# Performance work log

Measured on AMD Instinct MI355X. Metric: run time of the kernel, lower is better.

The kernel has to match this reference:

```python
import jax, jax.numpy as jnp
import numpy as np

IN_DIM = 128
OUT_DIM = 128
ATTN_DIM = 64
N_REL = 200
N_NODE = 50000
N_EDGE = 500000
N_QUERY = 64
COE_TIMEDIFF = 0.2  # computed in torch code but unused downstream


def setup_inputs() -> dict:
    key = jax.random.key(0)
    ks = jax.random.split(key, 24)
    # edges: [E,7] with columns (r_idx, _, rel, _, tau, sub, obj)
    r_idx = jax.random.randint(ks[0], (N_EDGE,), 0, N_QUERY)
    rel = jax.random.randint(ks[1], (N_EDGE,), 0, 2 * N_REL + 1)
    tau = jax.random.randint(ks[2], (N_EDGE,), -1, 366)  # -1 triggers the where() fallback
    sub = jax.random.randint(ks[3], (N_EDGE,), 0, N_NODE)
    obj = jax.random.randint(ks[4], (N_EDGE,), 0, N_NODE)
    fill = jnp.zeros((N_EDGE,), jnp.int64 if jax.config.jax_enable_x64 else jnp.int32)
    edges = jnp.stack([r_idx, fill, rel, fill, tau, sub, obj], axis=1)
    s = 1.0 / np.sqrt(IN_DIM)
    sa = 1.0 / np.sqrt(ATTN_DIM)
    return {
        "q_sub": jax.random.randint(ks[5], (N_QUERY,), 0, N_NODE),
        "q_rel": jax.random.randint(ks[6], (N_QUERY,), 0, 2 * N_REL + 1),
        "q_tau": jax.random.randint(ks[7], (N_QUERY,), 0, 366),
        "hidden": jax.random.normal(ks[8], (N_NODE, IN_DIM), jnp.float32),
        "edges": edges,
        "n_node": N_NODE,
        "old_nodes_new_idx": jax.random.randint(ks[9], (10000,), 0, N_NODE),
        "rela_embed": jax.random.normal(ks[10], (2 * N_REL + 1, IN_DIM), jnp.float32),
        "Ws": jax.random.normal(ks[11], (IN_DIM, ATTN_DIM), jnp.float32) * s,
        "Wr": jax.random.normal(ks[12], (IN_DIM, ATTN_DIM), jnp.float32) * s,
        "Wqr_W": jax.random.normal(ks[13], (IN_DIM, ATTN_DIM), jnp.float32) * s,
        "Wqr_b": jax.random.normal(ks[14], (ATTN_DIM,), jnp.float32) * s,
        "Wtau": jax.random.normal(ks[15], (IN_DIM, ATTN_DIM), jnp.float32) * s,
        "w_alpha_W": jax.random.normal(ks[16], (ATTN_DIM, 1), jnp.float32) * sa,
        "w_alpha_b": jax.random.normal(ks[17], (1,), jnp.float32) * sa,
        "Wh": jax.random.normal(ks[18], (IN_DIM, OUT_DIM), jnp.float32) * s,
        "wt1": jax.random.normal(ks[19], (1, IN_DIM), jnp.float32),
        "bt1": jax.random.normal(ks[20], (1, IN_DIM), jnp.float32),
        "wt2": jax.random.normal(ks[21], (1, IN_DIM), jnp.float32),
        "bt2": jax.random.normal(ks[22], (1, IN_DIM), jnp.float32),
    }


def reference(q_sub, q_rel, q_tau, hidden, edges, n_node, old_nodes_new_idx,
              rela_embed, Ws, Wr, Wqr_W, Wqr_b, Wtau, w_alpha_W, w_alpha_b,
              Wh, wt1, bt1, wt2, bt2):
    r_idx = edges[:, 0]
    rel = edges[:, 2]
    tau = edges[:, 4]
    sub = edges[:, 5]
    obj = edges[:, 6]
    hs = hidden[sub]                      # [E, in_dim] gather
    hr = rela_embed[rel]                  # [E, in_dim]
    h_qr = rela_embed[q_rel][r_idx]       # [E, in_dim]
    taus_q = q_tau[r_idx]
    tau = jnp.where(tau >= 0, tau, taus_q)
    delta_tau = (tau - taus_q).astype(hidden.dtype)[:, None]  # [E,1]
    h_tau = wt1 * delta_tau + bt1 + jnp.sin(wt2 * delta_tau + bt2)  # [E, in_dim]
    message = hs + hr + h_tau
    pre = jax.nn.relu(hs @ Ws + hr @ Wr + (h_qr @ Wqr_W + Wqr_b) + h_tau @ Wtau)
    alpha = jax.nn.sigmoid(pre @ w_alpha_W + w_alpha_b)  # [E,1]
    msg_agg = jax.ops.segment_sum(alpha * message, obj, num_segments=n_node)
    return msg_agg @ Wh  # act is identity by default
```

## Files before the change

kernel.cpp:

```cpp
#include <hip/hip_runtime.h>

#define IN_DIM   128
#define OUT_DIM  128
#define ATTN_DIM 64
#define N_RELV   401
#define N_NODE   50000
#define N_EDGE   500000
#define N_QUERY  64
#define N_DT     731
#define CAP      40

typedef unsigned short ushort_t;
typedef unsigned int   uint_t;
typedef __attribute__((ext_vector_type(8))) short v8s;
typedef __attribute__((ext_vector_type(4))) float v4f;

__device__ __forceinline__ int clampi(int v, int lo, int hi) {
    return v < lo ? lo : (v > hi ? hi : v);
}
__device__ __forceinline__ float bu2f(ushort_t u) {
    union { uint_t i; float f; } v; v.i = ((uint_t)u) << 16; return v.f;
}
__device__ __forceinline__ float blo(uint_t u) { return bu2f((ushort_t)(u & 0xffff)); }
__device__ __forceinline__ float bhi(uint_t u) { return bu2f((ushort_t)(u >> 16)); }
__device__ __forceinline__ ushort_t f2bu(float f) {
    union { float f; uint_t i; } v; v.f = f;
    const uint_t x = v.i;
    return (ushort_t)((x + 0x7fffu + ((x >> 16) & 1u)) >> 16);
}

__device__ __forceinline__ void parse_edge(const int* __restrict__ edges, int e,
                                           int i64, int& r, int& rel, int& tau,
                                           int& sub, int& obj) {
    if (i64) {
        const int* E = edges + (size_t)e * 14;
        r = E[0]; rel = E[4]; tau = E[8]; sub = E[10]; obj = E[12];
    } else {
        const int* E = edges + (size_t)e * 7;
        r = E[0]; rel = E[2]; tau = E[4]; sub = E[5]; obj = E[6];
    }
    r   = clampi(r,   0, N_QUERY - 1);
    rel = clampi(rel, 0, N_RELV - 1);
    sub = clampi(sub, 0, N_NODE - 1);
    obj = clampi(obj, 0, N_NODE - 1);
}

__global__ __launch_bounds__(256) void prep_kernel(
    const int* __restrict__ edges, const float* __restrict__ Ws,
    const float* __restrict__ Wh, ushort_t* __restrict__ WTb,
    int* __restrict__ flag, int* __restrict__ cnt, int* __restrict__ ovfn)
{
    const int i = blockIdx.x * 256 + threadIdx.x;
    const int n = i >> 7, k = i & 127;
    const float w = (n < 64) ? Ws[k * 64 + n] : Wh[k * 128 + (n - 64)];
    WTb[i] = f2bu(w);

    for (int idx = i; idx < N_NODE; idx += 96 * 256) cnt[idx] = 0;
    if (i == 0) ovfn[0] = 0;

    if (blockIdx.x == 0) {
        __shared__ int bad;
        if (threadIdx.x == 0) bad = 0;
        __syncthreads();
        for (int t = threadIdx.x; t < 1000; t += 256) {
            const int w32 = edges[2 * t + 1];
            if (w32 != 0 && w32 != -1) bad = 1;
        }
        __syncthreads();
        if (threadIdx.x == 0) flag[0] = (bad == 0) ? 1 : 0;
    }
}

__global__ __launch_bounds__(256) void node_tab_mfma(
    const float* __restrict__ hidden, const ushort_t* __restrict__ WTb,
    ushort_t* __restrict__ node_attn, ushort_t* __restrict__ node_msg)
{
    const int tid  = threadIdx.x;
    const int wid  = tid >> 6;
    const int lane = tid & 63;
    const int m16  = lane & 15;
    const int q    = lane >> 4;
    const int nb   = blockIdx.x * 64;
    const int row  = nb + wid * 16 + m16;
    const int rowc = row < N_NODE ? row : N_NODE - 1;

    v8s hfr[4];
    #pragma unroll
    for (int c = 0; c < 4; ++c) {
        const float4 f0 = *(const float4*)(hidden + (size_t)rowc * 128 + 32 * c + 8 * q);
        const float4 f1 = *(const float4*)(hidden + (size_t)rowc * 128 + 32 * c + 8 * q + 4);
        v8s a;
        a[0] = (short)f2bu(f0.x); a[1] = (short)f2bu(f0.y);
        a[2] = (short)f2bu(f0.z); a[3] = (short)f2bu(f0.w);
        a[4] = (short)f2bu(f1.x); a[5] = (short)f2bu(f1.y);
        a[6] = (short)f2bu(f1.z); a[7] = (short)f2bu(f1.w);
        hfr[c] = a;
    }

    #pragma unroll
    for (int t = 0; t < 12; ++t) {
        v4f acc = {0.f, 0.f, 0.f, 0.f};
        #pragma unroll
        for (int c = 0; c < 4; ++c) {
            const v8s wfr = *(const v8s*)(WTb + (size_t)(16 * t + m16) * 128 + 32 * c + 8 * q);
            acc = __builtin_amdgcn_mfma_f32_16x16x32_bf16(wfr, hfr[c], acc, 0, 0, 0);
        }
        if (row < N_NODE) {
            const uint_t u0 = (uint_t)f2bu(acc[0]) | ((uint_t)f2bu(acc[1]) << 16);
            const uint_t u1 = (uint_t)f2bu(acc[2]) | ((uint_t)f2bu(acc[3]) << 16);
            const int dim = 16 * t + 4 * q;
            if (dim < 64) {
                uint2* dst = (uint2*)(node_attn + (size_t)row * 64 + dim);
                *dst = make_uint2(u0, u1);
            } else {
                uint2* dst = (uint2*)(node_msg + (size_t)row * 128 + (dim - 64));
                *dst = make_uint2(u0, u1);
            }
        }
    }
}

__global__ __launch_bounds__(128) void tables_kernel(
    const float* __restrict__ rela, const float* __restrict__ Wr,
    const float* __restrict__ Wtau, const float* __restrict__ Wh,
    const float* __restrict__ wt1, const float* __restrict__ bt1,
    const float* __restrict__ wt2, const float* __restrict__ bt2,
    const int* __restrict__ q_rel, const float* __restrict__ WqrW,
    const float* __restrict__ Wqrb, const int* __restrict__ flag,
    ushort_t* __restrict__ rel_attn, ushort_t* __restrict__ rel_msg,
    ushort_t* __restrict__ dt_attn,  ushort_t* __restrict__ dt_msg,
    ushort_t* __restrict__ Xqr)
{
    const int b = blockIdx.x, tid = threadIdx.x;
    __shared__ float h[IN_DIM];

    if (b < N_RELV) {
        const int r = b;
        h[tid] = rela[(size_t)r * IN_DIM + tid];
        __syncthreads();
        if (tid < ATTN_DIM) {
            float a = 0.f;
            #pragma unroll 8
            for (int d = 0; d < IN_DIM; ++d) a += h[d] * Wr[d * ATTN_DIM + tid];
            rel_attn[(size_t)r * ATTN_DIM + tid] = f2bu(a);
        }
        float m = 0.f;
        #pragma unroll 8
        for (int d = 0; d < IN_DIM; ++d) m += h[d] * Wh[d * OUT_DIM + tid];
        rel_msg[(size_t)r * OUT_DIM + tid] = f2bu(m);
    } else if (b < N_RELV + N_DT) {
        const int i = b - N_RELV;
        const float dt = (float)(i - 365);
        h[tid] = wt1[tid] * dt + bt1[tid] + sinf(wt2[tid] * dt + bt2[tid]);
        __syncthreads();
        if (tid < ATTN_DIM) {
            float a = 0.f;
            #pragma unroll 8
            for (int d = 0; d < IN_DIM; ++d) a += h[d] * Wtau[d * ATTN_DIM + tid];
            dt_attn[(size_t)i * ATTN_DIM + tid] = f2bu(a);
        }
        float m = 0.f;
        #pragma unroll 8
        for (int d = 0; d < IN_DIM; ++d) m += h[d] * Wh[d * OUT_DIM + tid];
        dt_msg[(size_t)i * OUT_DIM + tid] = f2bu(m);
    } else {
        const int qn  = b - N_RELV - N_DT;
        const int i64 = flag[0];
        const int rel = clampi(q_rel[i64 ? 2 * qn : qn], 0, N_RELV - 1);
        h[tid] = rela[(size_t)rel * IN_DIM + tid];
        __syncthreads();
        if (tid < ATTN_DIM) {
            float acc = Wqrb[tid];
            #pragma unroll 8
            for (int d = 0; d < IN_DIM; ++d) acc += h[d] * WqrW[d * ATTN_DIM + tid];
            Xqr[(size_t)qn * ATTN_DIM + tid] = f2bu(acc);
        }
    }
}

__global__ __launch_bounds__(256) void alpha_scatter(
    const int* __restrict__ edges, const int* __restrict__ q_tau,
    const ushort_t* __restrict__ node_attn, const ushort_t* __restrict__ rel_attn,
    const ushort_t* __restrict__ dt_attn,  const ushort_t* __restrict__ Xqr,
    const float* __restrict__ w_alpha_W, const float* __restrict__ w_alpha_b,
    const int* __restrict__ flag, int* __restrict__ cnt,
    int4* __restrict__ meta, int* __restrict__ ovfn, int4* __restrict__ ovfl)
{
    const int g   = threadIdx.x & 7;
    const int e   = blockIdx.x * 32 + (threadIdx.x >> 3);
    const int i64 = flag[0];

    int r, rel, tau, sub, obj;
    parse_edge(edges, e, i64, r, rel, tau, sub, obj);
    const int tq = q_tau[i64 ? 2 * r : r];
    if (tau < 0) tau = tq;
    const int di = clampi(tau - tq + 365, 0, N_DT - 1);

    const uint4 xs = *(const uint4*)(node_attn + (size_t)sub * ATTN_DIM + 8 * g);
    const uint4 xr = *(const uint4*)(rel_attn + (size_t)rel * ATTN_DIM + 8 * g);
    const uint4 xt = *(const uint4*)(dt_attn  + (size_t)di  * ATTN_DIM + 8 * g);
    const uint4 xq = *(const uint4*)(Xqr      + (size_t)r   * ATTN_DIM + 8 * g);
    const float4 wA = *(const float4*)(w_alpha_W + 8 * g);
    const float4 wB = *(const float4*)(w_alpha_W + 8 * g + 4);

    float s0, s1, v;
    s0 = blo(xs.x) + blo(xr.x) + blo(xt.x) + blo(xq.x);
    s1 = bhi(xs.x) + bhi(xr.x) + bhi(xt.x) + bhi(xq.x);
    v  = fmaxf(s0, 0.f) * wA.x + fmaxf(s1, 0.f) * wA.y;
    s0 = blo(xs.y) + blo(xr.y) + blo(xt.y) + blo(xq.y);
    s1 = bhi(xs.y) + bhi(xr.y) + bhi(xt.y) + bhi(xq.y);
    v += fmaxf(s0, 0.f) * wA.z + fmaxf(s1, 0.f) * wA.w;
    s0 = blo(xs.z) + blo(xr.z) + blo(xt.z) + blo(xq.z);
    s1 = bhi(xs.z) + bhi(xr.z) + bhi(xt.z) + bhi(xq.z);
    v += fmaxf(s0, 0.f) * wB.x + fmaxf(s1, 0.f) * wB.y;
    s0 = blo(xs.w) + blo(xr.w) + blo(xt.w) + blo(xq.w);
    s1 = bhi(xs.w) + bhi(xr.w) + bhi(xt.w) + bhi(xq.w);
    v += fmaxf(s0, 0.f) * wB.z + fmaxf(s1, 0.f) * wB.w;

    v += __shfl_down(v, 4, 8);
    v += __shfl_down(v, 2, 8);
    v += __shfl_down(v, 1, 8);

    if (g == 0) {
        const float alpha = 1.f / (1.f + __expf(-(v + w_alpha_b[0])));
        const int pos = atomicAdd(&cnt[obj], 1);
        if (pos < CAP) {
            meta[(size_t)obj * CAP + pos] =
                make_int4(sub | (di << 17), rel, __float_as_int(alpha), 0);
        } else {
            const int ov = atomicAdd(ovfn, 1);
            if (ov < N_EDGE)
                ovfl[ov] = make_int4(sub | (di << 17), rel | (obj << 9),
                                     __float_as_int(alpha), 0);
        }
    }
}

__device__ __forceinline__ void agg_step(
    int4 m, int lane,
    const ushort_t* __restrict__ node_msg, const ushort_t* __restrict__ rel_msg,
    const ushort_t* __restrict__ dt_msg, float& a0, float& a1)
{
    const int sub = m.x & 0x1FFFF;
    const int di  = (int)(((uint_t)m.x) >> 17);
    const int rel = m.y;
    const float al = __int_as_float(m.z);
    const uint_t am = *(const uint_t*)(node_msg + (size_t)sub * 128 + 2 * lane);
    const uint_t bm = *(const uint_t*)(rel_msg  + (size_t)rel * 128 + 2 * lane);
    const uint_t tm = *(const uint_t*)(dt_msg   + (size_t)di  * 128 + 2 * lane);
    a0 += al * (blo(am) + blo(bm) + blo(tm));
    a1 += al * (bhi(am) + bhi(bm) + bhi(tm));
}

__global__ __launch_bounds__(256) void agg_kernel(
    const int* __restrict__ cnt, const int4* __restrict__ meta,
    const ushort_t* __restrict__ node_msg, const ushort_t* __restrict__ rel_msg,
    const ushort_t* __restrict__ dt_msg, float* __restrict__ out)
{
    const int lane = threadIdx.x & 63;
    const int n    = blockIdx.x * 4 + (threadIdx.x >> 6);

    int m = cnt[n]; if (m > CAP) m = CAP;
    const int4* row = meta + (size_t)n * CAP;
    float a0 = 0.f, a1 = 0.f;
    int j = 0;
    for (; j + 1 < m; j += 2) {
        const int4 m0 = row[j];
        const int4 m1 = row[j + 1];
        agg_step(m0, lane, node_msg, rel_msg, dt_msg, a0, a1);
        agg_step(m1, lane, node_msg, rel_msg, dt_msg, a0, a1);
    }
    if (j < m)
        agg_step(row[j], lane, node_msg, rel_msg, dt_msg, a0, a1);

    ((float2*)(out + (size_t)n * OUT_DIM))[lane] = make_float2(a0, a1);
}

__global__ __launch_bounds__(256) void ovf_fix(
    const int* __restrict__ ovfn, const int4* __restrict__ ovfl,
    const ushort_t* __restrict__ node_msg, const ushort_t* __restrict__ rel_msg,
    const ushort_t* __restrict__ dt_msg, float* __restrict__ out)
{
    const int lane = threadIdx.x & 63;
    int nov = ovfn[0]; if (nov > N_EDGE) nov = N_EDGE;
    for (int i = blockIdx.x * 4 + (threadIdx.x >> 6); i < nov; i += 64 * 4) {
        const int4 m = ovfl[i];
        const int sub = m.x & 0x1FFFF;
        const int di  = (int)(((uint_t)m.x) >> 17);
        const int rel = m.y & 0x1FF;
        const int obj = (int)(((uint_t)m.y) >> 9);
        const float al = __int_as_float(m.z);
        const uint_t am = *(const uint_t*)(node_msg + (size_t)sub * 128 + 2 * lane);
        const uint_t bm = *(const uint_t*)(rel_msg  + (size_t)rel * 128 + 2 * lane);
        const uint_t tm = *(const uint_t*)(dt_msg   + (size_t)di  * 128 + 2 * lane);
        float* dst = out + (size_t)obj * OUT_DIM;
        atomicAdd(dst + 2 * lane,     al * (blo(am) + blo(bm) + blo(tm)));
        atomicAdd(dst + 2 * lane + 1, al * (bhi(am) + bhi(bm) + bhi(tm)));
    }
}

__global__ __launch_bounds__(256) void edge_atomic_kernel(
    const int* __restrict__ edges, const int* __restrict__ q_tau,
    const ushort_t* __restrict__ node_attn, const ushort_t* __restrict__ node_msg,
    const ushort_t* __restrict__ rel_attn,  const ushort_t* __restrict__ rel_msg,
    const ushort_t* __restrict__ dt_attn,   const ushort_t* __restrict__ dt_msg,
    const ushort_t* __restrict__ Xqr,
    const float* __restrict__ w_alpha_W, const float* __restrict__ w_alpha_b,
    const int* __restrict__ flag, float* __restrict__ out)
{
    const int lane = threadIdx.x & 63;
    const int e    = blockIdx.x * 4 + (threadIdx.x >> 6);
    const int i64  = flag[0];

    int r, rel, tau, sub, obj;
    parse_edge(edges, e, i64, r, rel, tau, sub, obj);
    const int tq = q_tau[i64 ? 2 * r : r];
    if (tau < 0) tau = tq;
    const int di = clampi(tau - tq + 365, 0, N_DT - 1);

    const float xs = bu2f(node_attn[(size_t)sub * ATTN_DIM + lane]);
    const float xr = bu2f(rel_attn[(size_t)rel * ATTN_DIM + lane]);
    const float xt = bu2f(dt_attn[(size_t)di  * ATTN_DIM + lane]);
    const float xq = bu2f(Xqr[(size_t)r * ATTN_DIM + lane]);

    float v = fmaxf(xs + xr + xq + xt, 0.f) * w_alpha_W[lane];
    #pragma unroll
    for (int off = 32; off > 0; off >>= 1)
        v += __shfl_down(v, off, 64);
    v = __shfl(v, 0, 64);
    const float alpha = 1.f / (1.f + __expf(-(v + w_alpha_b[0])));

    const uint_t am = *(const uint_t*)(node_msg + (size_t)sub * 128 + 2 * lane);
    const uint_t bm = *(const uint_t*)(rel_msg  + (size_t)rel * 128 + 2 * lane);
    const uint_t tm = *(const uint_t*)(dt_msg   + (size_t)di  * 128 + 2 * lane);
    const float mx = blo(am) + blo(bm) + blo(tm);
    const float my = bhi(am) + bhi(bm) + bhi(tm);

    float* dst = out + (size_t)obj * OUT_DIM;
    atomicAdd(dst + 2 * lane,     alpha * mx);
    atomicAdd(dst + 2 * lane + 1, alpha * my);
}

extern "C" void kernel_launch(void* const* d_in, const int* in_sizes, int n_in,
                              void* d_out, int out_size, void* d_ws, size_t ws_size,
                              hipStream_t stream)
{
    const int*   q_rel  = (const int*)d_in[1];
    const int*   q_tau  = (const int*)d_in[2];
    const float* hidden = (const float*)d_in[3];
    const int*   edges  = (const int*)d_in[4];
    const float* rela   = (const float*)d_in[7];
    const float* Ws     = (const float*)d_in[8];
    const float* Wr     = (const float*)d_in[9];
    const float* WqrW   = (const float*)d_in[10];
    const float* Wqrb   = (const float*)d_in[11];
    const float* Wtau   = (const float*)d_in[12];
    const float* waW    = (const float*)d_in[13];
    const float* wab    = (const float*)d_in[14];
    const float* Wh     = (const float*)d_in[15];
    const float* wt1    = (const float*)d_in[16];
    const float* bt1    = (const float*)d_in[17];
    const float* wt2    = (const float*)d_in[18];
    const float* bt2    = (const float*)d_in[19];
    float* out = (float*)d_out;

    char* p = (char*)d_ws;
    size_t off = 0;
    auto carve = [&](size_t bytes) {
        char* q = p + off;
        off = (off + bytes + 255) & ~(size_t)255;
        return q;
    };
    int*      flag      = (int*)     carve(64);
    int*      cnt       = (int*)     carve((size_t)N_NODE * 4);
    int*      ovfn      = (int*)     carve(64);
    ushort_t* WTb       = (ushort_t*)carve((size_t)192 * 128 * 2);
    ushort_t* XqrB      = (ushort_t*)carve((size_t)N_QUERY * ATTN_DIM * 2);
    ushort_t* rel_attn  = (ushort_t*)carve((size_t)N_RELV * ATTN_DIM * 2);
    ushort_t* rel_msg   = (ushort_t*)carve((size_t)N_RELV * OUT_DIM * 2);
    ushort_t* dt_attn   = (ushort_t*)carve((size_t)N_DT * ATTN_DIM * 2);
    ushort_t* dt_msg    = (ushort_t*)carve((size_t)N_DT * OUT_DIM * 2);
    ushort_t* node_attn = (ushort_t*)carve((size_t)N_NODE * ATTN_DIM * 2);
    ushort_t* node_msg  = (ushort_t*)carve((size_t)N_NODE * OUT_DIM * 2);
    int4*     meta      = (int4*)    carve((size_t)N_NODE * CAP * 16);
    int4*     ovfl      = (int4*)    carve((size_t)N_EDGE * 16);
    const size_t need_full = off;

    prep_kernel<<<96, 256, 0, stream>>>(edges, Ws, Wh, WTb, flag, cnt, ovfn);
    tables_kernel<<<N_RELV + N_DT + N_QUERY, 128, 0, stream>>>(
        rela, Wr, Wtau, Wh, wt1, bt1, wt2, bt2, q_rel, WqrW, Wqrb, flag,
        rel_attn, rel_msg, dt_attn, dt_msg, XqrB);
    node_tab_mfma<<<(N_NODE + 63) / 64, 256, 0, stream>>>(hidden, WTb,
                                                          node_attn, node_msg);

    if (ws_size >= need_full) {
        alpha_scatter<<<N_EDGE / 32, 256, 0, stream>>>(edges, q_tau, node_attn,
                                                       rel_attn, dt_attn, XqrB,
                                                       waW, wab, flag, cnt,
                                                       meta, ovfn, ovfl);
        agg_kernel<<<N_NODE / 4, 256, 0, stream>>>(cnt, meta, node_msg,
                                                   rel_msg, dt_msg, out);
        ovf_fix<<<64, 256, 0, stream>>>(ovfn, ovfl, node_msg, rel_msg,
                                        dt_msg, out);
    } else {
        (void)hipMemsetAsync(out, 0, (size_t)out_size * sizeof(float), stream);
        edge_atomic_kernel<<<N_EDGE / 4, 256, 0, stream>>>(edges, q_tau,
                                                           node_attn, node_msg,
                                                           rel_attn, rel_msg,
                                                           dt_attn, dt_msg, XqrB,
                                                           waW, wab, flag, out);
    }
}
```

Baseline: 229.6 us.

## Pack edge metadata to 8 bytes, fold overflow fix into aggregation, batch edges

Edge metadata records shrink from int4 to int2: the relation index is split across both words and alpha is stored as fp16. This halves scatter and gather traffic on the per-node buckets. alpha_scatter now handles two edges per 8-lane group, and agg_kernel unrolls by four to overlap more gathers. The separate ovf_fix kernel is removed, and each node instead scans the full overflow list. That scan is cheap when the list is empty but costs O(nodes x overflow) when it is not, and fp16 alpha reduces precision.

```diff
diff --git a/kernel.cpp b/kernel.cpp
--- a/kernel.cpp
+++ b/kernel.cpp
@@ -1,4 +1,5 @@
 #include <hip/hip_runtime.h>
+#include <hip/hip_fp16.h>
 
 #define IN_DIM   128
 #define OUT_DIM  128
@@ -178,31 +179,9 @@
     }
 }
 
-__global__ __launch_bounds__(256) void alpha_scatter(
-    const int* __restrict__ edges, const int* __restrict__ q_tau,
-    const ushort_t* __restrict__ node_attn, const ushort_t* __restrict__ rel_attn,
-    const ushort_t* __restrict__ dt_attn,  const ushort_t* __restrict__ Xqr,
-    const float* __restrict__ w_alpha_W, const float* __restrict__ w_alpha_b,
-    const int* __restrict__ flag, int* __restrict__ cnt,
-    int4* __restrict__ meta, int* __restrict__ ovfn, int4* __restrict__ ovfl)
-{
-    const int g   = threadIdx.x & 7;
-    const int e   = blockIdx.x * 32 + (threadIdx.x >> 3);
-    const int i64 = flag[0];
-
-    int r, rel, tau, sub, obj;
-    parse_edge(edges, e, i64, r, rel, tau, sub, obj);
-    const int tq = q_tau[i64 ? 2 * r : r];
-    if (tau < 0) tau = tq;
-    const int di = clampi(tau - tq + 365, 0, N_DT - 1);
-
-    const uint4 xs = *(const uint4*)(node_attn + (size_t)sub * ATTN_DIM + 8 * g);
-    const uint4 xr = *(const uint4*)(rel_attn + (size_t)rel * ATTN_DIM + 8 * g);
-    const uint4 xt = *(const uint4*)(dt_attn  + (size_t)di  * ATTN_DIM + 8 * g);
-    const uint4 xq = *(const uint4*)(Xqr      + (size_t)r   * ATTN_DIM + 8 * g);
-    const float4 wA = *(const float4*)(w_alpha_W + 8 * g);
-    const float4 wB = *(const float4*)(w_alpha_W + 8 * g + 4);
-
+__device__ __forceinline__ float dot8(uint4 xs, uint4 xr, uint4 xt, uint4 xq,
+                                      float4 wA, float4 wB)
+{
     float s0, s1, v;
     s0 = blo(xs.x) + blo(xr.x) + blo(xt.x) + blo(xq.x);
     s1 = bhi(xs.x) + bhi(xr.x) + bhi(xt.x) + bhi(xq.x);
@@ -216,87 +195,167 @@
     s0 = blo(xs.w) + blo(xr.w) + blo(xt.w) + blo(xq.w);
     s1 = bhi(xs.w) + bhi(xr.w) + bhi(xt.w) + bhi(xq.w);
     v += fmaxf(s0, 0.f) * wB.z + fmaxf(s1, 0.f) * wB.w;
-
-    v += __shfl_down(v, 4, 8);
-    v += __shfl_down(v, 2, 8);
-    v += __shfl_down(v, 1, 8);
+    return v;
+}
+
+__global__ __launch_bounds__(256) void alpha_scatter(
+    const int* __restrict__ edges, const int* __restrict__ q_tau,
+    const ushort_t* __restrict__ node_attn, const ushort_t* __restrict__ rel_attn,
+    const ushort_t* __restrict__ dt_attn,  const ushort_t* __restrict__ Xqr,
+    const float* __restrict__ w_alpha_W, const float* __restrict__ w_alpha_b,
+    const int* __restrict__ flag, int* __restrict__ cnt,
+    int2* __restrict__ meta, int* __restrict__ ovfn, int4* __restrict__ ovfl)
+{
+    const int g   = threadIdx.x & 7;
+    const int grp = threadIdx.x >> 3;
+    const int e0  = blockIdx.x * 64 + grp * 2;
+    const int i64 = flag[0];
+
+    const float4 wA = *(const float4*)(w_alpha_W + 8 * g);
+    const float4 wB = *(const float4*)(w_alpha_W + 8 * g + 4);
+
+    const int ea = e0     < N_EDGE ? e0     : N_EDGE - 1;
+    const int eb = e0 + 1 < N_EDGE ? e0 + 1 : N_EDGE - 1;
+
+    int r0, rel0, tau0, sub0, obj0, r1, rel1, tau1, sub1, obj1;
+    parse_edge(edges, ea, i64, r0, rel0, tau0, sub0, obj0);
+    parse_edge(edges, eb, i64, r1, rel1, tau1, sub1, obj1);
+    const int tq0 = q_tau[i64 ? 2 * r0 : r0];
+    const int tq1 = q_tau[i64 ? 2 * r1 : r1];
+    if (tau0 < 0) tau0 = tq0;
+    if (tau1 < 0) tau1 = tq1;
+    const int di0 = clampi(tau0 - tq0 + 365, 0, N_DT - 1);
+    const int di1 = clampi(tau1 - tq1 + 365, 0, N_DT - 1);
+
+    const uint4 xs0 = *(const uint4*)(node_attn + (size_t)sub0 * ATTN_DIM + 8 * g);
+    const uint4 xr0 = *(const uint4*)(rel_attn + (size_t)rel0 * ATTN_DIM + 8 * g);
+    const uint4 xt0 = *(const uint4*)(dt_attn  + (size_t)di0  * ATTN_DIM + 8 * g);
+    const uint4 xq0 = *(const uint4*)(Xqr      + (size_t)r0   * ATTN_DIM + 8 * g);
+    const uint4 xs1 = *(const uint4*)(node_attn + (size_t)sub1 * ATTN_DIM + 8 * g);
+    const uint4 xr1 = *(const uint4*)(rel_attn + (size_t)rel1 * ATTN_DIM + 8 * g);
+    const uint4 xt1 = *(const uint4*)(dt_attn  + (size_t)di1  * ATTN_DIM + 8 * g);
+    const uint4 xq1 = *(const uint4*)(Xqr      + (size_t)r1   * ATTN_DIM + 8 * g);
+
+    float v0 = dot8(xs0, xr0, xt0, xq0, wA, wB);
+    float v1 = dot8(xs1, xr1, xt1, xq1, wA, wB);
+    v0 += __shfl_down(v0, 4, 8);
+    v1 += __shfl_down(v1, 4, 8);
+    v0 += __shfl_down(v0, 2, 8);
+    v1 += __shfl_down(v1, 2, 8);
+    v0 += __shfl_down(v0, 1, 8);
+    v1 += __shfl_down(v1, 1, 8);
 
     if (g == 0) {
-        const float alpha = 1.f / (1.f + __expf(-(v + w_alpha_b[0])));
-        const int pos = atomicAdd(&cnt[obj], 1);
-        if (pos < CAP) {
-            meta[(size_t)obj * CAP + pos] =
-                make_int4(sub | (di << 17), rel, __float_as_int(alpha), 0);
-        } else {
-            const int ov = atomicAdd(ovfn, 1);
-            if (ov < N_EDGE)
-                ovfl[ov] = make_int4(sub | (di << 17), rel | (obj << 9),
-                                     __float_as_int(alpha), 0);
-        }
-    }
-}
-
-__device__ __forceinline__ void agg_step(
-    int4 m, int lane,
-    const ushort_t* __restrict__ node_msg, const ushort_t* __restrict__ rel_msg,
-    const ushort_t* __restrict__ dt_msg, float& a0, float& a1)
-{
-    const int sub = m.x & 0x1FFFF;
-    const int di  = (int)(((uint_t)m.x) >> 17);
-    const int rel = m.y;
-    const float al = __int_as_float(m.z);
-    const uint_t am = *(const uint_t*)(node_msg + (size_t)sub * 128 + 2 * lane);
-    const uint_t bm = *(const uint_t*)(rel_msg  + (size_t)rel * 128 + 2 * lane);
-    const uint_t tm = *(const uint_t*)(dt_msg   + (size_t)di  * 128 + 2 * lane);
-    a0 += al * (blo(am) + blo(bm) + blo(tm));
-    a1 += al * (bhi(am) + bhi(bm) + bhi(tm));
+        const float wb = w_alpha_b[0];
+        if (e0 < N_EDGE) {
+            const float alpha = 1.f / (1.f + __expf(-(v0 + wb)));
+            const int pos = atomicAdd(&cnt[obj0], 1);
+            if (pos < CAP) {
+                const uint_t px = (uint_t)sub0 | ((uint_t)di0 << 17) | ((uint_t)(rel0 & 31) << 27);
+                const uint_t py = (uint_t)(rel0 >> 5) |
+                                  ((uint_t)__half_as_ushort(__float2half_rn(alpha)) << 16);
+                meta[(size_t)obj0 * CAP + pos] = make_int2((int)px, (int)py);
+            } else {
+                const int ov = atomicAdd(ovfn, 1);
+                if (ov < N_EDGE)
+                    ovfl[ov] = make_int4(sub0 | (di0 << 17), rel0 | (obj0 << 9),
+                                         __float_as_int(alpha), 0);
+            }
+        }
+        if (e0 + 1 < N_EDGE) {
+            const float alpha = 1.f / (1.f + __expf(-(v1 + wb)));
+            const int pos = atomicAdd(&cnt[obj1], 1);
+            if (pos < CAP) {
+                const uint_t px = (uint_t)sub1 | ((uint_t)di1 << 17) | ((uint_t)(rel1 & 31) << 27);
+                const uint_t py = (uint_t)(rel1 >> 5) |
+                                  ((uint_t)__half_as_ushort(__float2half_rn(alpha)) << 16);
+                meta[(size_t)obj1 * CAP + pos] = make_int2((int)px, (int)py);
+            } else {
+                const int ov = atomicAdd(ovfn, 1);
+                if (ov < N_EDGE)
+                    ovfl[ov] = make_int4(sub1 | (di1 << 17), rel1 | (obj1 << 9),
+                                         __float_as_int(alpha), 0);
+            }
+        }
+    }
+}
+
+__device__ __forceinline__ void meta_decode(int2 m, int& sub, int& di, int& rel,
+                                            float& al)
+{
+    sub = m.x & 0x1FFFF;
+    di  = ((uint_t)m.x >> 17) & 0x3FF;
+    rel = (((uint_t)m.x >> 27) & 31) | (((uint_t)m.y & 0xF) << 5);
+    al  = __half2float(__ushort_as_half((ushort_t)((uint_t)m.y >> 16)));
 }
 
 __global__ __launch_bounds__(256) void agg_kernel(
-    const int* __restrict__ cnt, const int4* __restrict__ meta,
-    const ushort_t* __restrict__ node_msg, const ushort_t* __restrict__ rel_msg,
-    const ushort_t* __restrict__ dt_msg, float* __restrict__ out)
-{
-    const int lane = threadIdx.x & 63;
-    const int n    = blockIdx.x * 4 + (threadIdx.x >> 6);
-
-    int m = cnt[n]; if (m > CAP) m = CAP;
-    const int4* row = meta + (size_t)n * CAP;
-    float a0 = 0.f, a1 = 0.f;
-    int j = 0;
-    for (; j + 1 < m; j += 2) {
-        const int4 m0 = row[j];
-        const int4 m1 = row[j + 1];
-        agg_step(m0, lane, node_msg, rel_msg, dt_msg, a0, a1);
-        agg_step(m1, lane, node_msg, rel_msg, dt_msg, a0, a1);
-    }
-    if (j < m)
-        agg_step(row[j], lane, node_msg, rel_msg, dt_msg, a0, a1);
-
-    ((float2*)(out + (size_t)n * OUT_DIM))[lane] = make_float2(a0, a1);
-}
-
-__global__ __launch_bounds__(256) void ovf_fix(
+    const int* __restrict__ cnt, const int2* __restrict__ meta,
     const int* __restrict__ ovfn, const int4* __restrict__ ovfl,
     const ushort_t* __restrict__ node_msg, const ushort_t* __restrict__ rel_msg,
     const ushort_t* __restrict__ dt_msg, float* __restrict__ out)
 {
     const int lane = threadIdx.x & 63;
+    const int n    = blockIdx.x * 4 + (threadIdx.x >> 6);
+
+    int m = cnt[n]; if (m > CAP) m = CAP;
+    const int2* row = meta + (size_t)n * CAP;
+    float a0 = 0.f, a1 = 0.f;
+    int j = 0;
+    for (; j + 3 < m; j += 4) {
+        const int2 m0 = row[j], m1 = row[j + 1], m2 = row[j + 2], m3 = row[j + 3];
+        int s0, d0, r0; float w0; meta_decode(m0, s0, d0, r0, w0);
+        int s1, d1, r1; float w1; meta_decode(m1, s1, d1, r1, w1);
+        int s2, d2, r2; float w2; meta_decode(m2, s2, d2, r2, w2);
+        int s3, d3, r3; float w3; meta_decode(m3, s3, d3, r3, w3);
+        const uint_t am0 = *(const uint_t*)(node_msg + (size_t)s0 * 128 + 2 * lane);
+        const uint_t bm0 = *(const uint_t*)(rel_msg  + (size_t)r0 * 128 + 2 * lane);
+        const uint_t tm0 = *(const uint_t*)(dt_msg   + (size_t)d0 * 128 + 2 * lane);
+        const uint_t am1 = *(const uint_t*)(node_msg + (size_t)s1 * 128 + 2 * lane);
+        const uint_t bm1 = *(const uint_t*)(rel_msg  + (size_t)r1 * 128 + 2 * lane);
+        const uint_t tm1 = *(const uint_t*)(dt_msg   + (size_t)d1 * 128 + 2 * lane);
+        const uint_t am2 = *(const uint_t*)(node_msg + (size_t)s2 * 128 + 2 * lane);
+        const uint_t bm2 = *(const uint_t*)(rel_msg  + (size_t)r2 * 128 + 2 * lane);
+        const uint_t tm2 = *(const uint_t*)(dt_msg   + (size_t)d2 * 128 + 2 * lane);
+        const uint_t am3 = *(const uint_t*)(node_msg + (size_t)s3 * 128 + 2 * lane);
+        const uint_t bm3 = *(const uint_t*)(rel_msg  + (size_t)r3 * 128 + 2 * lane);
+        const uint_t tm3 = *(const uint_t*)(dt_msg   + (size_t)d3 * 128 + 2 * lane);
+        a0 += w0 * (blo(am0) + blo(bm0) + blo(tm0));
+        a1 += w0 * (bhi(am0) + bhi(bm0) + bhi(tm0));
+        a0 += w1 * (blo(am1) + blo(bm1) + blo(tm1));
+        a1 += w1 * (bhi(am1) + bhi(bm1) + bhi(tm1));
+        a0 += w2 * (blo(am2) + blo(bm2) + blo(tm2));
+        a1 += w2 * (bhi(am2) + bhi(bm2) + bhi(tm2));
+        a0 += w3 * (blo(am3) + blo(bm3) + blo(tm3));
+        a1 += w3 * (bhi(am3) + bhi(bm3) + bhi(tm3));
+    }
+    for (; j < m; ++j) {
+        const int2 m0 = row[j];
+        int s0, d0, r0; float w0; meta_decode(m0, s0, d0, r0, w0);
+        const uint_t am0 = *(const uint_t*)(node_msg + (size_t)s0 * 128 + 2 * lane);
+        const uint_t bm0 = *(const uint_t*)(rel_msg  + (size_t)r0 * 128 + 2 * lane);
+        const uint_t tm0 = *(const uint_t*)(dt_msg   + (size_t)d0 * 128 + 2 * lane);
+        a0 += w0 * (blo(am0) + blo(bm0) + blo(tm0));
+        a1 += w0 * (bhi(am0) + bhi(bm0) + bhi(tm0));
+    }
+
     int nov = ovfn[0]; if (nov > N_EDGE) nov = N_EDGE;
-    for (int i = blockIdx.x * 4 + (threadIdx.x >> 6); i < nov; i += 64 * 4) {
-        const int4 m = ovfl[i];
-        const int sub = m.x & 0x1FFFF;
-        const int di  = (int)(((uint_t)m.x) >> 17);
-        const int rel = m.y & 0x1FF;
-        const int obj = (int)(((uint_t)m.y) >> 9);
-        const float al = __int_as_float(m.z);
-        const uint_t am = *(const uint_t*)(node_msg + (size_t)sub * 128 + 2 * lane);
-        const uint_t bm = *(const uint_t*)(rel_msg  + (size_t)rel * 128 + 2 * lane);
-        const uint_t tm = *(const uint_t*)(dt_msg   + (size_t)di  * 128 + 2 * lane);
-        float* dst = out + (size_t)obj * OUT_DIM;
-        atomicAdd(dst + 2 * lane,     al * (blo(am) + blo(bm) + blo(tm)));
-        atomicAdd(dst + 2 * lane + 1, al * (bhi(am) + bhi(bm) + bhi(tm)));
-    }
+    for (int i = 0; i < nov; ++i) {
+        const int4 mo = ovfl[i];
+        const int objo = (int)((uint_t)mo.y >> 9);
+        if (objo != n) continue;
+        const int subo = mo.x & 0x1FFFF;
+        const int dio  = (int)((uint_t)mo.x >> 17);
+        const int relo = mo.y & 0x1FF;
+        const float alo = __int_as_float(mo.z);
+        const uint_t am = *(const uint_t*)(node_msg + (size_t)subo * 128 + 2 * lane);
+        const uint_t bm = *(const uint_t*)(rel_msg  + (size_t)relo * 128 + 2 * lane);
+        const uint_t tm = *(const uint_t*)(dt_msg   + (size_t)dio  * 128 + 2 * lane);
+        a0 += alo * (blo(am) + blo(bm) + blo(tm));
+        a1 += alo * (bhi(am) + bhi(bm) + bhi(tm));
+    }
+
+    ((float2*)(out + (size_t)n * OUT_DIM))[lane] = make_float2(a0, a1);
 }
 
 __global__ __launch_bounds__(256) void edge_atomic_kernel(
@@ -382,7 +441,7 @@
     ushort_t* dt_msg    = (ushort_t*)carve((size_t)N_DT * OUT_DIM * 2);
     ushort_t* node_attn = (ushort_t*)carve((size_t)N_NODE * ATTN_DIM * 2);
     ushort_t* node_msg  = (ushort_t*)carve((size_t)N_NODE * OUT_DIM * 2);
-    int4*     meta      = (int4*)    carve((size_t)N_NODE * CAP * 16);
+    int2*     meta      = (int2*)    carve((size_t)N_NODE * CAP * 8);
     int4*     ovfl      = (int4*)    carve((size_t)N_EDGE * 16);
     const size_t need_full = off;
 
@@ -394,14 +453,11 @@
                                                           node_attn, node_msg);
 
     if (ws_size >= need_full) {
-        alpha_scatter<<<N_EDGE / 32, 256, 0, stream>>>(edges, q_tau, node_attn,
-                                                       rel_attn, dt_attn, XqrB,
-                                                       waW, wab, flag, cnt,
-                                                       meta, ovfn, ovfl);
-        agg_kernel<<<N_NODE / 4, 256, 0, stream>>>(cnt, meta, node_msg,
-                                                   rel_msg, dt_msg, out);
-        ovf_fix<<<64, 256, 0, stream>>>(ovfn, ovfl, node_msg, rel_msg,
-                                        dt_msg, out);
+        alpha_scatter<<<(N_EDGE + 63) / 64, 256, 0, stream>>>(
+            edges, q_tau, node_attn, rel_attn, dt_attn, XqrB,
+            waW, wab, flag, cnt, meta, ovfn, ovfl);
+        agg_kernel<<<N_NODE / 4, 256, 0, stream>>>(cnt, meta, ovfn, ovfl,
+                                                   node_msg, rel_msg, dt_msg, out);
     } else {
         (void)hipMemsetAsync(out, 0, (size_t)out_size * sizeof(float), stream);
         edge_atomic_kernel<<<N_EDGE / 4, 256, 0, stream>>>(edges, q_tau,
```

Result: faster. 217.1 us (-5.4%).
